# Kernel tuning notes

Measured on AMD Instinct MI355X. Metric: run time of the kernel, lower is better.

The kernel has to match this reference:

```python
import jax, jax.numpy as jnp
from jax import lax
import numpy as np

SHAPE = (50, 60, 65)   # -> after net: (17, 27, 32), flatten = 14688
NEG = 0.01             # LeakyReLU default slope
B, N = 8, 80000        # batch size, total active voxels


def _lrelu(x):
    return jnp.where(x >= 0, x, NEG * x)


def _sparse_conv(x, w, b, m):
    # Regular (non-submanifold) sparse conv == dense VALID conv on densified
    # input (inactive sites are 0 so they contribute nothing). Output site is
    # active iff any input site in the kernel footprint is active; bias is
    # added only at active output sites.
    k = w.shape[2]
    y = lax.conv_general_dilated(x, w, (1, 1, 1), 'VALID',
                                 dimension_numbers=('NCDHW', 'OIDHW', 'NCDHW'))
    m2 = lax.reduce_window(m, 0.0, lax.max, (1, 1, k, k, k), (1, 1, 1, 1, 1), 'VALID')
    y = jnp.where(m2 > 0, y + b[None, :, None, None, None], 0.0)
    return y, m2


def _sparse_maxpool(x, m, k):
    # spconv SparseMaxPool: max over ACTIVE sites only (inactive excluded, not 0)
    xm = jnp.where(m > 0, x, -jnp.inf)
    p = lax.reduce_window(xm, -jnp.inf, lax.max, (1, 1, k, k, k), (1, 1, 1, 1, 1), 'VALID')
    m2 = lax.reduce_window(m, 0.0, lax.max, (1, 1, k, k, k), (1, 1, 1, 1, 1), 'VALID')
    return jnp.where(m2 > 0, p, 0.0), m2


def setup_inputs() -> dict:
    key = jax.random.key(0)
    ks = jax.random.split(key, 24)
    D, H, W = SHAPE
    features = jax.random.normal(ks[0], (N, 1), dtype=jnp.float32)
    bi = jax.random.randint(ks[1], (N,), 0, B)
    zi = jax.random.randint(ks[2], (N,), 0, D)
    yi = jax.random.randint(ks[3], (N,), 0, H)
    xi = jax.random.randint(ks[4], (N,), 0, W)
    coors = jnp.stack([bi, zi, yi, xi], axis=1).astype(jnp.int32)
    s = 0.05
    p = {}
    p['w1'] = jax.random.normal(ks[5], (32, 1, 4, 4, 4), jnp.float32) * s
    p['b1'] = jax.random.normal(ks[6], (32,), jnp.float32) * s
    p['w2'] = jax.random.normal(ks[7], (32, 32, 4, 4, 4), jnp.float32) * s
    p['b2'] = jax.random.normal(ks[8], (32,), jnp.float32) * s
    p['w3'] = jax.random.normal(ks[9], (32, 32, 4, 4, 4), jnp.float32) * s
    p['b3'] = jax.random.normal(ks[10], (32,), jnp.float32) * s
    p['w4'] = jax.random.normal(ks[11], (32, 32, 4, 4, 4), jnp.float32) * s
    p['b4'] = jax.random.normal(ks[12], (32,), jnp.float32) * s
    p['w5'] = jax.random.normal(ks[13], (32, 32, 4, 4, 4), jnp.float32) * s
    p['b5'] = jax.random.normal(ks[14], (32,), jnp.float32) * s
    p['w6'] = jax.random.normal(ks[15], (32, 32, 4, 4, 4), jnp.float32) * s
    p['b6'] = jax.random.normal(ks[16], (32,), jnp.float32) * s
    p['w7'] = jax.random.normal(ks[17], (1, 32, 4, 4, 4), jnp.float32) * s
    p['b7'] = jax.random.normal(ks[18], (1,), jnp.float32) * s
    p['W8'] = jax.random.normal(ks[19], (14688, 1000), jnp.float32) * 0.01
    p['b8'] = jax.random.normal(ks[20], (1000,), jnp.float32) * s
    p['W9'] = jax.random.normal(ks[21], (1000, 1000), jnp.float32) * 0.03
    p['b9'] = jax.random.normal(ks[22], (1000,), jnp.float32) * s
    p['W10'] = jax.random.normal(ks[23], (1000, 1), jnp.float32) * 0.03
    p['b10'] = jnp.zeros((1,), jnp.float32)
    return dict(features=features, coors=coors, batch_size=B, **p)


def reference(features, coors, batch_size,
              w1, b1, w2, b2, w3, b3, w4, b4, w5, b5, w6, b6, w7, b7,
              W8, b8, W9, b9, W10, b10):
    D, H, W = SHAPE
    bi, zi, yi, xi = coors[:, 0], coors[:, 1], coors[:, 2], coors[:, 3]
    dense = jnp.zeros((batch_size, 1, D, H, W), features.dtype)
    dense = dense.at[bi, 0, zi, yi, xi].set(features[:, 0])
    mask = jnp.zeros((batch_size, 1, D, H, W), features.dtype)
    mask = mask.at[bi, 0, zi, yi, xi].set(1.0)

    x, m = _sparse_conv(dense, w1, b1, mask); x = _lrelu(x)
    x, m = _sparse_conv(x, w2, b2, m);        x = _lrelu(x)
    x, m = _sparse_maxpool(x, m, 5)
    x, m = _sparse_conv(x, w3, b3, m);        x = _lrelu(x)
    x, m = _sparse_conv(x, w4, b4, m);        x = _lrelu(x)
    x, m = _sparse_maxpool(x, m, 5)
    x, m = _sparse_conv(x, w5, b5, m);        x = _lrelu(x)
    x, m = _sparse_conv(x, w6, b6, m);        x = _lrelu(x)
    x, m = _sparse_conv(x, w7, b7, m);        x = _lrelu(x)
    x, m = _sparse_maxpool(x, m, 5)

    # ToDense (inactive sites already 0) + Flatten -> [B, 14688]
    h = x.reshape(x.shape[0], -1)
    h = _lrelu(h @ W8 + b8)
    h = _lrelu(h @ W9 + b9)
    out = _lrelu(h @ W10 + b10)
    return out
```

## Files before the change

### kernel.cpp

```cpp
#include <hip/hip_runtime.h>
#include <cstddef>


#define NEGSLOPE 0.01f
#define NINF (-3.0e38f)

#define TZ 4
#define TY 4
#define TXT 16
#define IZ 7
#define IY 7
#define IX 19
#define NV (IZ*IY*IX)

#define CZ 4
#define CY 4
#define CX 8
#define HIY 7
#define HIX 11
#define HNV (7*HIY*HIX)

typedef __attribute__((ext_vector_type(8)))  short  short8;
typedef __attribute__((ext_vector_type(16))) float  floatx16;

__device__ __forceinline__ float lrelu(float v) { return v >= 0.f ? v : NEGSLOPE * v; }

__device__ __forceinline__ unsigned short f2bf(float f) {
  unsigned b = __float_as_uint(f);
  return (unsigned short)((b + 0x7fffu + ((b >> 16) & 1u)) >> 16);
}
__device__ __forceinline__ float bf2f(unsigned short h) {
  return __uint_as_float(((unsigned)h) << 16);
}
__device__ __forceinline__ unsigned splitpair(float a, float b, unsigned& lo) {
  unsigned short ha = f2bf(a), hb = f2bf(b);
  unsigned short la = f2bf(a - bf2f(ha)), lb = f2bf(b - bf2f(hb));
  lo = (unsigned)la | ((unsigned)lb << 16);
  return (unsigned)ha | ((unsigned)hb << 16);
}

__global__ void k_claim(const int* __restrict__ coors, unsigned* __restrict__ claim, int N) {
  int i = blockIdx.x * blockDim.x + threadIdx.x;
  if (i >= N) return;
  int b = coors[4*i], z = coors[4*i+1], y = coors[4*i+2], x = coors[4*i+3];
  int v = ((b*50 + z)*60 + y)*65 + x;
  atomicMax(&claim[v], (unsigned)(i + 1));
}

__global__ void k_scatter(const int* __restrict__ coors, const float* __restrict__ feat,
                          const unsigned* __restrict__ claim,
                          float* __restrict__ x0, float* __restrict__ m0, int N) {
  int i = blockIdx.x * blockDim.x + threadIdx.x;
  if (i >= N) return;
  int b = coors[4*i], z = coors[4*i+1], y = coors[4*i+2], x = coors[4*i+3];
  int v = ((b*50 + z)*60 + y)*65 + x;
  m0[v] = 1.f;
  if (claim[v] == (unsigned)(i + 1)) x0[v] = feat[i];
}

__global__ void k_repack(const float* __restrict__ w, float* __restrict__ wr, int CI, int CO) {
  int i = blockIdx.x * blockDim.x + threadIdx.x;
  int tot = CO * CI * 64;
  if (i >= tot) return;
  int k = i & 63;
  int ci = (i >> 6) % CI;
  int co = i / (64 * CI);
  wr[(k * CI + ci) * CO + co] = w[i];
}

__global__ void k_repack_mfma(const float* __restrict__ w, unsigned short* __restrict__ tbl) {
  int i = blockIdx.x * blockDim.x + threadIdx.x;
  if (i >= 64*4*2*64) return;
  int lane = i & 63; int t = i >> 6;
  int pack = t & 1; t >>= 1;
  int pass = t & 3; int tap = t >> 2;
  int co = lane & 31; int oct = lane >> 5;
#pragma unroll
  for (int j = 0; j < 8; ++j) {
    int k = oct * 8 + j;
    int ci = pass * 8 + (k & 7);
    int part = ((k >> 3) ^ pack) & 1;
    float wv = w[((co * 32 + ci) << 6) + tap];
    unsigned short wh = f2bf(wv);
    unsigned short r = part ? f2bf(wv - bf2f(wh)) : wh;
    tbl[(size_t)i * 8 + j] = r;
  }
}

__global__ void kd_z(const float* __restrict__ in, float* __restrict__ o,
                     int Zi, int Yi, int Xi, int Zo, int K, int nI) {
  int gid = blockIdx.x * blockDim.x + threadIdx.x;
  int perOut = Zo * Yi * Xi;
  if (gid >= nI * perOut) return;
  int item = gid / perOut;
  int r = gid - item * perOut;
  int x = r % Xi; int t = r / Xi;
  int y = t % Yi; int z = t / Yi;
  const float* ib = in + (size_t)item * Zi * Yi * Xi;
  float mx = 0.f;
  for (int d = 0; d < K; d++) mx = fmaxf(mx, ib[((z + d) * Yi + y) * Xi + x]);
  o[gid] = mx;
}

__global__ void kd_y(const float* __restrict__ in, float* __restrict__ o,
                     int Zo, int Yi, int Xi, int Yo, int K, int nI) {
  int gid = blockIdx.x * blockDim.x + threadIdx.x;
  int perOut = Zo * Yo * Xi;
  if (gid >= nI * perOut) return;
  int item = gid / perOut;
  int r = gid - item * perOut;
  int x = r % Xi; int t = r / Xi;
  int y = t % Yo; int z = t / Yo;
  const float* ib = in + (size_t)item * Zo * Yi * Xi;
  float mx = 0.f;
  for (int d = 0; d < K; d++) mx = fmaxf(mx, ib[(z * Yi + y + d) * Xi + x]);
  o[gid] = mx;
}

__global__ void kd_x(const float* __restrict__ in, float* __restrict__ o,
                     int Zo, int Yo, int Xi, int Xo, int K, int nI) {
  int gid = blockIdx.x * blockDim.x + threadIdx.x;
  int perOut = Zo * Yo * Xo;
  if (gid >= nI * perOut) return;
  int item = gid / perOut;
  int r = gid - item * perOut;
  int x = r % Xo; int t = r / Xo;
  int y = t % Yo; int z = t / Yo;
  const float* ib = in + (size_t)item * Zo * Yo * Xi;
  float mx = 0.f;
  for (int d = 0; d < K; d++) mx = fmaxf(mx, ib[(z * Yo + y) * Xi + x + d]);
  o[gid] = mx;
}

__global__ __launch_bounds__(256, 6)
void k_conv32m(const float* __restrict__ in, const unsigned short* __restrict__ tbl,
               const float* __restrict__ bias, const float* __restrict__ mo,
               float* __restrict__ out,
               int Zi, int Yi, int Xi, int Zo, int Yo, int Xo,
               int tilesZ, int tilesY, int tilesX) {
  __shared__ unsigned sU[HNV * 12];
  const int perIn = Zi * Yi * Xi;
  const int perOut = Zo * Yo * Xo;
  int bid = blockIdx.x;
  int txi = bid % tilesX; bid /= tilesX;
  int tyi = bid % tilesY; bid /= tilesY;
  int tzi = bid % tilesZ; int item = bid / tilesZ;
  const int z0 = tzi * CZ, y0 = tyi * CY, x0 = txi * CX;
  const int tid = threadIdx.x;
  const int lane = tid & 63;
  const int col = lane & 31;
  const int oct = lane >> 5;
  const int wv  = tid >> 6;

  const int lvBase = ((wv) * HIY + ((col >> 3) & 3)) * HIX + (col & 7);

  floatx16 acc;
#pragma unroll
  for (int r = 0; r < 16; ++r) acc[r] = 0.f;

  const float* inb = in + (size_t)item * perIn * 32;
  const char* tb = (const char*)tbl + lane * 16;

#pragma unroll 1
  for (int p = 0; p < 4; ++p) {
    __syncthreads();
    for (int idx = tid; idx < HNV; idx += 256) {
      int iz = idx / (HIY * HIX); int r = idx - iz * (HIY * HIX);
      int iy = r / HIX; int ix = r - iy * HIX;
      int gz = z0 + iz, gy = y0 + iy, gx = x0 + ix;
      float4 f0 = make_float4(0.f,0.f,0.f,0.f), f1 = make_float4(0.f,0.f,0.f,0.f);
      if (gz < Zi && gy < Yi && gx < Xi) {
        const float* vp = inb + (size_t)((gz * Yi + gy) * Xi + gx) * 32 + p * 8;
        f0 = *(const float4*)vp;
        f1 = *(const float4*)(vp + 4);
      }
      unsigned l0, l1, l2, l3;
      unsigned h0 = splitpair(f0.x, f0.y, l0);
      unsigned h1 = splitpair(f0.z, f0.w, l1);
      unsigned h2 = splitpair(f1.x, f1.y, l2);
      unsigned h3 = splitpair(f1.z, f1.w, l3);
      uint4 ahv = {h0, h1, h2, h3};
      uint4 alv = {l0, l1, l2, l3};
      ((uint4*)sU)[idx * 3 + 0] = ahv;
      ((uint4*)sU)[idx * 3 + 1] = alv;
    }
    __syncthreads();

    const char* tp = tb + (size_t)p * 2048;
#pragma unroll 2
    for (int tap = 0; tap < 64; ++tap) {
      int kz = tap >> 4, ky = (tap >> 2) & 3, kx = tap & 3;
      int sOff = (kz * HIY + ky) * HIX + kx;
      short8 b0 = *(const short8*)(tp + (size_t)tap * 8192);
      short8 b1 = *(const short8*)(tp + (size_t)tap * 8192 + 1024);
      short8 a0 = *(const short8*)((const char*)sU + (size_t)(lvBase + sOff) * 48 + oct * 16);
      acc = __builtin_amdgcn_mfma_f32_32x32x16_bf16(a0, b0, acc, 0, 0, 0);
      acc = __builtin_amdgcn_mfma_f32_32x32x16_bf16(a0, b1, acc, 0, 0, 0);
    }
  }

  const float bco = bias[col];
#pragma unroll
  for (int rg = 0; rg < 16; ++rg) {
    int row = (rg & 3) + 8 * (rg >> 2) + 4 * oct;
    int oz = wv, oy = (row >> 3) & 3, ox = row & 7;
    int gz = z0 + oz, gy = y0 + oy, gx = x0 + ox;
    if (gz < Zo && gy < Yo && gx < Xo) {
      int ov = item * perOut + (gz * Yo + gy) * Xo + gx;
      bool act = mo[ov] > 0.f;
      out[(size_t)ov * 32 + col] = lrelu(act ? (acc[rg] + bco) : 0.f);
    }
  }
}

__global__ __launch_bounds__(256, 2)
void k_conv1t(const float* __restrict__ in, const float* __restrict__ wr,
              const float* __restrict__ bias, const float* __restrict__ mo,
              float* __restrict__ out,
              int Zi, int Yi, int Xi, int Zo, int Yo, int Xo,
              int tilesZ, int tilesY, int tilesX) {
  __shared__ float sinf[NV];
  __shared__ float4 wsh[512];
  {
    const float4* wr4 = (const float4*)wr;
    for (int idx = threadIdx.x; idx < 512; idx += 256) wsh[idx] = wr4[idx];
  }
  const int perIn = Zi * Yi * Xi;
  const int perOut = Zo * Yo * Xo;
  int bid = blockIdx.x;
  int txi = bid % tilesX; bid /= tilesX;
  int tyi = bid % tilesY; bid /= tilesY;
  int tzi = bid % tilesZ; int item = bid / tilesZ;
  const int z0 = tzi * TZ, y0 = tyi * TY, x0 = txi * TXT;
  const int tid = threadIdx.x;
  const int ox = tid & 15, oy = (tid >> 4) & 3, oz = tid >> 6;

  const float* inb = in + (size_t)item * perIn;
  for (int idx = tid; idx < NV; idx += 256) {
    int iz = idx / (IY * IX); int r = idx - iz * (IY * IX);
    int iy = r / IX; int ix = r - iy * IX;
    int gz = z0 + iz, gy = y0 + iy, gx = x0 + ix;
    float val = 0.f;
    if (gz < Zi && gy < Yi && gx < Xi)
      val = inb[(size_t)((gz * Yi + gy) * Xi + gx)];
    sinf[idx] = val;
  }
  __syncthreads();

  float4 acc[8];
#pragma unroll
  for (int j = 0; j < 8; ++j) acc[j] = make_float4(0.f, 0.f, 0.f, 0.f);

#pragma unroll 1
  for (int tap = 0; tap < 64; ++tap) {
    int kz = tap >> 4, ky = (tap >> 2) & 3, kx = tap & 3;
    int lv = ((oz + kz) * IY + (oy + ky)) * IX + (ox + kx);
    float av = sinf[lv];
#pragma unroll
    for (int j = 0; j < 8; ++j) {
      float4 wvv = wsh[tap * 8 + j];
      acc[j].x = fmaf(av, wvv.x, acc[j].x);
      acc[j].y = fmaf(av, wvv.y, acc[j].y);
      acc[j].z = fmaf(av, wvv.z, acc[j].z);
      acc[j].w = fmaf(av, wvv.w, acc[j].w);
    }
  }

  int gz = z0 + oz, gy = y0 + oy, gx = x0 + ox;
  if (gz < Zo && gy < Yo && gx < Xo) {
    int ov = item * perOut + (gz * Yo + gy) * Xo + gx;
    bool act = mo[ov] > 0.f;
    const float4* b4 = (const float4*)bias;
    float* op = out + (size_t)ov * 32;
#pragma unroll
    for (int j = 0; j < 8; ++j) {
      float4 r = acc[j]; float4 bj = b4[j];
      r.x = lrelu(act ? (r.x + bj.x) : 0.f);
      r.y = lrelu(act ? (r.y + bj.y) : 0.f);
      r.z = lrelu(act ? (r.z + bj.z) : 0.f);
      r.w = lrelu(act ? (r.w + bj.w) : 0.f);
      *(float4*)(op + j * 4) = r;
    }
  }
}

__global__ __launch_bounds__(256, 2)
void k_conv7t(const float* __restrict__ in, const float* __restrict__ wr,
              const float* __restrict__ bias, const float* __restrict__ mo,
              float* __restrict__ out,
              int Zi, int Yi, int Xi, int Zo, int Yo, int Xo,
              int tilesZ, int tilesY, int tilesX) {
  __shared__ float4 sin4[4][NV];
  __shared__ float4 wsh[512];
  {
    const float4* wr4 = (const float4*)wr;
    for (int idx = threadIdx.x; idx < 512; idx += 256) wsh[idx] = wr4[idx];
  }
  const int perIn = Zi * Yi * Xi;
  const int perOut = Zo * Yo * Xo;
  int bid = blockIdx.x;
  int txi = bid % tilesX; bid /= tilesX;
  int tyi = bid % tilesY; bid /= tilesY;
  int tzi = bid % tilesZ; int item = bid / tilesZ;
  const int z0 = tzi * TZ, y0 = tyi * TY, x0 = txi * TXT;
  const int tid = threadIdx.x;
  const int ox = tid & 15, oy = (tid >> 4) & 3, oz = tid >> 6;

  const float* inb = in + (size_t)item * perIn * 32;
  float acc = 0.f;

#pragma unroll 1
  for (int h = 0; h < 2; ++h) {
    __syncthreads();
    for (int idx = tid; idx < NV * 4; idx += 256) {
      int q = idx / NV; int v = idx - q * NV;
      int iz = v / (IY * IX); int r = v - iz * (IY * IX);
      int iy = r / IX; int ix = r - iy * IX;
      int gz = z0 + iz, gy = y0 + iy, gx = x0 + ix;
      float4 val = make_float4(0.f, 0.f, 0.f, 0.f);
      if (gz < Zi && gy < Yi && gx < Xi)
        val = *(const float4*)(inb + (size_t)((gz * Yi + gy) * Xi + gx) * 32 + h * 16 + q * 4);
      sin4[q][v] = val;
    }
    __syncthreads();
#pragma unroll 1
    for (int tap = 0; tap < 64; ++tap) {
      int kz = tap >> 4, ky = (tap >> 2) & 3, kx = tap & 3;
      int lv = ((oz + kz) * IY + (oy + ky)) * IX + (ox + kx);
      float4 a0 = sin4[0][lv];
      float4 a1 = sin4[1][lv];
      float4 a2 = sin4[2][lv];
      float4 a3 = sin4[3][lv];
      float4 w0 = wsh[tap * 8 + h * 4 + 0];
      float4 w1 = wsh[tap * 8 + h * 4 + 1];
      float4 w2 = wsh[tap * 8 + h * 4 + 2];
      float4 w3 = wsh[tap * 8 + h * 4 + 3];
      acc += a0.x*w0.x + a0.y*w0.y + a0.z*w0.z + a0.w*w0.w
           + a1.x*w1.x + a1.y*w1.y + a1.z*w1.z + a1.w*w1.w
           + a2.x*w2.x + a2.y*w2.y + a2.z*w2.z + a2.w*w2.w
           + a3.x*w3.x + a3.y*w3.y + a3.z*w3.z + a3.w*w3.w;
    }
  }

  int gz = z0 + oz, gy = y0 + oy, gx = x0 + ox;
  if (gz < Zo && gy < Yo && gx < Xo) {
    int ov = item * perOut + (gz * Yo + gy) * Xo + gx;
    bool act = mo[ov] > 0.f;
    out[ov] = lrelu(act ? (acc + bias[0]) : 0.f);
  }
}

__global__ void k_pool_z(const float* __restrict__ in, const float* __restrict__ m,
                         float* __restrict__ out, int Zi, int Yi, int Xi, int Zo, int nI) {
  int gid = blockIdx.x * blockDim.x + threadIdx.x;
  int perOut = Zo * Yi * Xi;
  int tot = nI * perOut * 8;
  if (gid >= tot) return;
  int c4 = gid & 7; int v = gid >> 3;
  int item = v / perOut;
  int r = v - item * perOut;
  int x = r % Xi; int t = r / Xi;
  int y = t % Yi; int z = t / Yi;
  int ib = item * Zi * Yi * Xi;
  float4 acc = {NINF, NINF, NINF, NINF};
  for (int j = 0; j < 5; j++) {
    int vi = ib + ((z + j)*Yi + y)*Xi + x;
    if (m[vi] > 0.f) {
      float4 val = *(const float4*)(in + (size_t)vi*32 + c4*4);
      acc.x = fmaxf(acc.x, val.x); acc.y = fmaxf(acc.y, val.y);
      acc.z = fmaxf(acc.z, val.z); acc.w = fmaxf(acc.w, val.w);
    }
  }
  *(float4*)(out + (size_t)v*32 + c4*4) = acc;
}

__global__ void k_pool_y(const float* __restrict__ in, float* __restrict__ out,
                         int Z, int Yi, int Xi, int Yo, int nI) {
  int gid = blockIdx.x * blockDim.x + threadIdx.x;
  int perOut = Z * Yo * Xi;
  int tot = nI * perOut * 8;
  if (gid >= tot) return;
  int c4 = gid & 7; int v = gid >> 3;
  int item = v / perOut;
  int r = v - item * perOut;
  int x = r % Xi; int t = r / Xi;
  int y = t % Yo; int z = t / Yo;
  int ib = item * Z * Yi * Xi;
  float4 acc = {NINF, NINF, NINF, NINF};
  for (int j = 0; j < 5; j++) {
    int vi = ib + (z*Yi + y + j)*Xi + x;
    float4 val = *(const float4*)(in + (size_t)vi*32 + c4*4);
    acc.x = fmaxf(acc.x, val.x); acc.y = fmaxf(acc.y, val.y);
    acc.z = fmaxf(acc.z, val.z); acc.w = fmaxf(acc.w, val.w);
  }
  *(float4*)(out + (size_t)v*32 + c4*4) = acc;
}

__global__ void k_pool_x(const float* __restrict__ in, const float* __restrict__ mp,
                         float* __restrict__ out, int Z, int Y, int Xi, int Xo, int nI) {
  int gid = blockIdx.x * blockDim.x + threadIdx.x;
  int perOut = Z * Y * Xo;
  int tot = nI * perOut * 8;
  if (gid >= tot) return;
  int c4 = gid & 7; int v = gid >> 3;
  int item = v / perOut;
  int r = v - item * perOut;
  int x = r % Xo; int t = r / Xo;
  int y = t % Y; int z = t / Y;
  int ib = item * Z * Y * Xi;
  float4 acc = {NINF, NINF, NINF, NINF};
  for (int j = 0; j < 5; j++) {
    int vi = ib + (z*Y + y)*Xi + x + j;
    float4 val = *(const float4*)(in + (size_t)vi*32 + c4*4);
    acc.x = fmaxf(acc.x, val.x); acc.y = fmaxf(acc.y, val.y);
    acc.z = fmaxf(acc.z, val.z); acc.w = fmaxf(acc.w, val.w);
  }
  bool act = mp[v] > 0.f;
  float4 rr;
  rr.x = act ? acc.x : 0.f; rr.y = act ? acc.y : 0.f;
  rr.z = act ? acc.z : 0.f; rr.w = act ? acc.w : 0.f;
  *(float4*)(out + (size_t)v*32 + c4*4) = rr;
}

__global__ void k_pool3(const float* __restrict__ xin, const float* __restrict__ m,
                        const float* __restrict__ mp, float* __restrict__ out, int nI) {
  int gid = blockIdx.x * blockDim.x + threadIdx.x;
  int perOut = 17 * 27 * 32;
  int tot = nI * perOut;
  if (gid >= tot) return;
  int item = gid / perOut;
  int r = gid - item * perOut;
  int x = r & 31; int t = r >> 5;
  int y = t % 27; int z = t / 27;
  const float* xb = xin + (size_t)item * 23436;
  const float* mb = m + (size_t)item * 23436;
  float acc = NINF;
  for (int dz = 0; dz < 5; dz++)
    for (int dy = 0; dy < 5; dy++) {
      const float* rowx = xb + (size_t)(((z + dz)*31 + y + dy)*36 + x);
      const float* rowm = mb + (size_t)(((z + dz)*31 + y + dy)*36 + x);
      for (int dx = 0; dx < 5; dx++)
        if (rowm[dx] > 0.f) acc = fmaxf(acc, rowx[dx]);
    }
  out[gid] = (mp[gid] > 0.f) ? acc : 0.f;
}

__global__ __launch_bounds__(256, 4)
void k_fc_part(const float* __restrict__ X, const float* __restrict__ Wm,
               float* __restrict__ part, int K, int Ncol, int Kc) {
  __shared__ float sm[16][16][8];
  int ks = blockIdx.y;
  int k0 = ks * Kc;
  int k1 = k0 + Kc; if (k1 > K) k1 = K;
  int cl = threadIdx.x & 15;
  int kt = threadIdx.x >> 4;
  int col = blockIdx.x * 16 + cl;
  float a0=0.f,a1=0.f,a2=0.f,a3=0.f,a4=0.f,a5=0.f,a6=0.f,a7=0.f;
  if (col < Ncol) {
    for (int k = k0 + kt; k < k1; k += 16) {
      float w = Wm[(size_t)k * Ncol + col];
      a0 += X[0 * K + k] * w; a1 += X[1 * K + k] * w;
      a2 += X[2 * K + k] * w; a3 += X[3 * K + k] * w;
      a4 += X[4 * K + k] * w; a5 += X[5 * K + k] * w;
      a6 += X[6 * K + k] * w; a7 += X[7 * K + k] * w;
    }
  }
  sm[kt][cl][0]=a0; sm[kt][cl][1]=a1; sm[kt][cl][2]=a2; sm[kt][cl][3]=a3;
  sm[kt][cl][4]=a4; sm[kt][cl][5]=a5; sm[kt][cl][6]=a6; sm[kt][cl][7]=a7;
  __syncthreads();
  if (threadIdx.x < 128) {
    int c = threadIdx.x & 15;
    int b = threadIdx.x >> 4;
    float s = 0.f;
#pragma unroll
    for (int k = 0; k < 16; k++) s += sm[k][c][b];
    int cc = blockIdx.x * 16 + c;
    if (cc < Ncol) part[((size_t)ks * 8 + b) * Ncol + cc] = s;
  }
}

__global__ void k_fc_fin(const float* __restrict__ part, int ns,
                         const float* __restrict__ bias, float* __restrict__ out, int Ncol) {
  int i = blockIdx.x * blockDim.x + threadIdx.x;
  if (i >= 8 * Ncol) return;
  int b = i / Ncol;
  int c = i - b * Ncol;
  float s = 0.f;
  for (int ks = 0; ks < ns; ks++) s += part[((size_t)ks * 8 + b) * Ncol + c];
  out[i] = lrelu(s + bias[c]);
}

__global__ __launch_bounds__(256, 4)
void k_fc(const float* __restrict__ X, const float* __restrict__ Wm,
          const float* __restrict__ bias, float* __restrict__ out,
          int K, int Ncol) {
  __shared__ float sm[16][16][8];
  int cl = threadIdx.x & 15;
  int kt = threadIdx.x >> 4;
  int col = blockIdx.x * 16 + cl;
  float a0=0.f,a1=0.f,a2=0.f,a3=0.f,a4=0.f,a5=0.f,a6=0.f,a7=0.f;
  if (col < Ncol) {
    for (int k = kt; k < K; k += 16) {
      float w = Wm[(size_t)k * Ncol + col];
      a0 += X[0 * K + k] * w; a1 += X[1 * K + k] * w;
      a2 += X[2 * K + k] * w; a3 += X[3 * K + k] * w;
      a4 += X[4 * K + k] * w; a5 += X[5 * K + k] * w;
      a6 += X[6 * K + k] * w; a7 += X[7 * K + k] * w;
    }
  }
  sm[kt][cl][0]=a0; sm[kt][cl][1]=a1; sm[kt][cl][2]=a2; sm[kt][cl][3]=a3;
  sm[kt][cl][4]=a4; sm[kt][cl][5]=a5; sm[kt][cl][6]=a6; sm[kt][cl][7]=a7;
  __syncthreads();
  if (threadIdx.x < 128) {
    int c = threadIdx.x & 15;
    int b = threadIdx.x >> 4;
    float s = 0.f;
#pragma unroll
    for (int k = 0; k < 16; k++) s += sm[k][c][b];
    int cc = blockIdx.x * 16 + c;
    if (cc < Ncol) out[b * Ncol + cc] = lrelu(s + bias[cc]);
  }
}

static inline int G256(long long n) { return (int)((n + 255) / 256); }

extern "C" void kernel_launch(void* const* d_in, const int* in_sizes, int n_in,
                              void* d_out, int out_size, void* d_ws, size_t ws_size,
                              hipStream_t stream) {
  const float* feat  = (const float*)d_in[0];
  const int*   coors = (const int*)d_in[1];
  const float* w1 = (const float*)d_in[3];  const float* b1 = (const float*)d_in[4];
  const float* w2 = (const float*)d_in[5];  const float* b2 = (const float*)d_in[6];
  const float* w3 = (const float*)d_in[7];  const float* b3 = (const float*)d_in[8];
  const float* w4 = (const float*)d_in[9];  const float* b4 = (const float*)d_in[10];
  const float* w5 = (const float*)d_in[11]; const float* b5 = (const float*)d_in[12];
  const float* w6 = (const float*)d_in[13]; const float* b6 = (const float*)d_in[14];
  const float* w7 = (const float*)d_in[15]; const float* b7 = (const float*)d_in[16];
  const float* W8 = (const float*)d_in[17]; const float* b8 = (const float*)d_in[18];
  const float* W9 = (const float*)d_in[19]; const float* b9 = (const float*)d_in[20];
  const float* W10= (const float*)d_in[21]; const float* b10= (const float*)d_in[22];
  float* out = (float*)d_out;

  char* ws = (char*)d_ws;
  size_t off = 0;
  auto alloc = [&](size_t nfloats) -> float* {
    float* p = (float*)(ws + off);
    off += ((nfloats * 4 + 1023) / 1024) * 1024;
    return p;
  };

  float* x0  = alloc(1560000);
  float* m0  = alloc(1560000);
  float* m1  = alloc(8 * 166098);
  float* m2  = alloc(8 * 140184);
  float* mp1 = alloc(8 * 110000);
  float* m3  = alloc(8 * 90428);
  float* m4  = alloc(8 * 73304);
  float* mp2 = alloc(8 * 54000);
  float* m5  = alloc(8 * 41958);
  float* m6  = alloc(8 * 31824);
  float* m7  = alloc(8 * 23436);
  float* mp3 = alloc(8 * 14688);
  float* p3  = alloc(8 * 14688);
  float* dt1 = alloc(8 * 183300);
  float* dt2 = alloc(8 * 174135);
  float* wr1 = alloc(2048);
  float* wr7 = alloc(2048);
  unsigned short* tb2 = (unsigned short*)alloc(131072);
  unsigned short* tb3 = (unsigned short*)alloc(131072);
  unsigned short* tb4 = (unsigned short*)alloc(131072);
  unsigned short* tb5 = (unsigned short*)alloc(131072);
  unsigned short* tb6 = (unsigned short*)alloc(131072);
  float* part= alloc(64000);
  float* h8  = alloc(8000);
  float* h9  = alloc(8000);
  size_t fixedOff = off;

  const size_t perItemAB = ((size_t)5315136*4 + 1023)/1024*1024
                         + ((size_t)4485888*4 + 1023)/1024*1024
                         + ((size_t)23436*4 + 1023)/1024*1024;
  int G = 0;
  for (int g : {8, 4, 2, 1})
    if (fixedOff + (size_t)g * perItemAB <= ws_size) { G = g; break; }
  if (G == 0) return;

  float* A  = alloc((size_t)G * 5315136);
  float* Bb = alloc((size_t)G * 4485888);
  float* x7 = alloc((size_t)G * 23436);
  unsigned* claim = (unsigned*)A;

  hipMemsetAsync(claim, 0, 1560000 * 4, stream);
  hipMemsetAsync(x0,    0, 1560000 * 4, stream);
  hipMemsetAsync(m0,    0, 1560000 * 4, stream);

  k_repack<<<G256(32*1*64),  256, 0, stream>>>(w1, wr1, 1, 32);
  k_repack<<<G256(1*32*64),  256, 0, stream>>>(w7, wr7, 32, 1);
  k_repack_mfma<<<128, 256, 0, stream>>>(w2, tb2);
  k_repack_mfma<<<128, 256, 0, stream>>>(w3, tb3);
  k_repack_mfma<<<128, 256, 0, stream>>>(w4, tb4);
  k_repack_mfma<<<128, 256, 0, stream>>>(w5, tb5);
  k_repack_mfma<<<128, 256, 0, stream>>>(w6, tb6);

  const int N = 80000;
  k_claim  <<<G256(N), 256, 0, stream>>>(coors, claim, N);
  k_scatter<<<G256(N), 256, 0, stream>>>(coors, feat, claim, x0, m0, N);

  auto dil3 = [&](const float* src, float* dst,
                  int Zi, int Yi, int Xi, int Zo, int Yo, int Xo, int K) {
    kd_z<<<G256((long long)8*Zo*Yi*Xi), 256, 0, stream>>>(src, dt1, Zi,Yi,Xi, Zo, K, 8);
    kd_y<<<G256((long long)8*Zo*Yo*Xi), 256, 0, stream>>>(dt1, dt2, Zo,Yi,Xi, Yo, K, 8);
    kd_x<<<G256((long long)8*Zo*Yo*Xo), 256, 0, stream>>>(dt2, dst, Zo,Yo,Xi, Xo, K, 8);
  };
  dil3(m0,  m1,  50,60,65, 47,57,62, 4);
  dil3(m1,  m2,  47,57,62, 44,54,59, 4);
  dil3(m2,  mp1, 44,54,59, 40,50,55, 5);
  dil3(mp1, m3,  40,50,55, 37,47,52, 4);
  dil3(m3,  m4,  37,47,52, 34,44,49, 4);
  dil3(m4,  mp2, 34,44,49, 30,40,45, 5);
  dil3(mp2, m5,  30,40,45, 27,37,42, 4);
  dil3(m5,  m6,  27,37,42, 24,34,39, 4);
  dil3(m6,  m7,  24,34,39, 21,31,36, 4);
  dil3(m7,  mp3, 21,31,36, 17,27,32, 5);

  auto conv32 = [&](const float* in, const unsigned short* tbl, const float* bias,
                    const float* mo, float* o,
                    int Zi, int Yi, int Xi, int Zo, int Yo, int Xo, int nI) {
    int tz = (Zo + CZ - 1) / CZ, ty = (Yo + CY - 1) / CY, tx = (Xo + CX - 1) / CX;
    k_conv32m<<<nI * tz * ty * tx, 256, 0, stream>>>(
        in, tbl, bias, mo, o, Zi, Yi, Xi, Zo, Yo, Xo, tz, ty, tx);
  };

  for (int g0 = 0; g0 < 8; g0 += G) {
    const float* x0g  = x0  + (size_t)g0 * 195000;
    const float* m1g  = m1  + (size_t)g0 * 166098;
    const float* m2g  = m2  + (size_t)g0 * 140184;
    const float* mp1g = mp1 + (size_t)g0 * 110000;
    const float* m3g  = m3  + (size_t)g0 * 90428;
    const float* m4g  = m4  + (size_t)g0 * 73304;
    const float* mp2g = mp2 + (size_t)g0 * 54000;
    const float* m5g  = m5  + (size_t)g0 * 41958;
    const float* m6g  = m6  + (size_t)g0 * 31824;
    const float* m7g  = m7  + (size_t)g0 * 23436;
    const float* mp3g = mp3 + (size_t)g0 * 14688;

    {
      int tz = (47 + TZ - 1) / TZ, ty = (57 + TY - 1) / TY, tx = (62 + TXT - 1) / TXT;
      k_conv1t<<<G * tz * ty * tx, 256, 0, stream>>>(
          x0g, wr1, b1, m1g, A, 50,60,65, 47,57,62, tz, ty, tx);
    }
    conv32(A, tb2, b2, m2g, Bb, 47,57,62, 44,54,59, G);
    k_pool_z<<<G256((long long)G*127440*8), 256, 0, stream>>>(Bb, m2g,  A,  44,54,59, 40, G);
    k_pool_y<<<G256((long long)G*118000*8), 256, 0, stream>>>(A,  Bb, 40,54,59, 50, G);
    k_pool_x<<<G256((long long)G*110000*8), 256, 0, stream>>>(Bb, mp1g, A,  40,50,59, 55, G);
    conv32(A, tb3, b3, m3g, Bb, 40,50,55, 37,47,52, G);
    conv32(Bb, tb4, b4, m4g, A, 37,47,52, 34,44,49, G);
    k_pool_z<<<G256((long long)G*64680*8), 256, 0, stream>>>(A,  m4g,  Bb, 34,44,49, 30, G);
    k_pool_y<<<G256((long long)G*58800*8), 256, 0, stream>>>(Bb, A,  30,44,49, 40, G);
    k_pool_x<<<G256((long long)G*54000*8), 256, 0, stream>>>(A,  mp2g, Bb, 30,40,49, 45, G);
    conv32(Bb, tb5, b5, m5g, A, 30,40,45, 27,37,42, G);
    conv32(A, tb6, b6, m6g, Bb, 27,37,42, 24,34,39, G);
    {
      int tz = (21 + TZ - 1) / TZ, ty = (31 + TY - 1) / TY, tx = (36 + TXT - 1) / TXT;
      k_conv7t<<<G * tz * ty * tx, 256, 0, stream>>>(
          Bb, wr7, b7, m7g, x7, 24,34,39, 21,31,36, tz, ty, tx);
    }
    k_pool3<<<G256((long long)G*14688), 256, 0, stream>>>(
        x7, m7g, mp3g, p3 + (size_t)g0 * 14688, G);
  }

  k_fc_part<<<dim3(63, 8), 256, 0, stream>>>(p3, W8, part, 14688, 1000, 1836);
  k_fc_fin <<<G256(8000), 256, 0, stream>>>(part, 8, b8, h8, 1000);
  k_fc_part<<<dim3(63, 4), 256, 0, stream>>>(h8, W9, part, 1000, 1000, 250);
  k_fc_fin <<<G256(8000), 256, 0, stream>>>(part, 4, b9, h9, 1000);
  k_fc<<<1, 256, 0, stream>>>(h9, W10, b10, out, 1000, 1);
}
```

Before: 3.574 ms.

## Double output tile per block in MFMA conv, reuse B fragments across two accumulators

The 32-channel conv kernel now covers a 4x4x16 output tile per block instead of 4x4x8. Each wave holds two 32-row accumulators, so each loaded weight fragment feeds four MFMAs instead of two. The shared-memory stride per voxel drops from 48 to 40 bytes, written and read as uint2 pairs to cut padding and bank conflicts. The goal is less redundant halo loading and bf16 splitting per output, and more MFMA work per weight load, at the cost of more registers (occupancy hint lowered from 6 to 4) and more wasted tiles at the X edges.

```diff
diff --git a/kernel.cpp b/kernel.cpp
--- a/kernel.cpp
+++ b/kernel.cpp
@@ -13,15 +13,9 @@
 #define IX 19
 #define NV (IZ*IY*IX)
 
-#define CZ 4
-#define CY 4
-#define CX 8
-#define HIY 7
-#define HIX 11
-#define HNV (7*HIY*HIX)
-
-typedef __attribute__((ext_vector_type(8)))  short  short8;
-typedef __attribute__((ext_vector_type(16))) float  floatx16;
+typedef __attribute__((ext_vector_type(8)))  short    short8;
+typedef __attribute__((ext_vector_type(4)))  unsigned uint4v;
+typedef __attribute__((ext_vector_type(16))) float    floatx16;
 
 __device__ __forceinline__ float lrelu(float v) { return v >= 0.f ? v : NEGSLOPE * v; }
 
@@ -37,6 +31,13 @@
   unsigned short la = f2bf(a - bf2f(ha)), lb = f2bf(b - bf2f(hb));
   lo = (unsigned)la | ((unsigned)lb << 16);
   return (unsigned)ha | ((unsigned)hb << 16);
+}
+
+__device__ __forceinline__ short8 ld_frag(const uint2* s2, int v, int oct) {
+  uint2 u0 = s2[v * 5 + oct * 2];
+  uint2 u1 = s2[v * 5 + oct * 2 + 1];
+  uint4v t; t.x = u0.x; t.y = u0.y; t.z = u1.x; t.w = u1.y;
+  return __builtin_bit_cast(short8, t);
 }
 
 __global__ void k_claim(const int* __restrict__ coors, unsigned* __restrict__ claim, int N) {
@@ -132,41 +133,48 @@
   o[gid] = mx;
 }
 
-__global__ __launch_bounds__(256, 6)
+__global__ __launch_bounds__(256, 4)
 void k_conv32m(const float* __restrict__ in, const unsigned short* __restrict__ tbl,
                const float* __restrict__ bias, const float* __restrict__ mo,
                float* __restrict__ out,
                int Zi, int Yi, int Xi, int Zo, int Yo, int Xo,
                int tilesZ, int tilesY, int tilesX) {
-  __shared__ unsigned sU[HNV * 12];
+  __shared__ unsigned sU[NV * 10];
   const int perIn = Zi * Yi * Xi;
   const int perOut = Zo * Yo * Xo;
   int bid = blockIdx.x;
   int txi = bid % tilesX; bid /= tilesX;
   int tyi = bid % tilesY; bid /= tilesY;
   int tzi = bid % tilesZ; int item = bid / tilesZ;
-  const int z0 = tzi * CZ, y0 = tyi * CY, x0 = txi * CX;
+  const int z0 = tzi * TZ, y0 = tyi * TY, x0 = txi * TXT;
   const int tid = threadIdx.x;
   const int lane = tid & 63;
   const int col = lane & 31;
   const int oct = lane >> 5;
   const int wv  = tid >> 6;
 
-  const int lvBase = ((wv) * HIY + ((col >> 3) & 3)) * HIX + (col & 7);
-
-  floatx16 acc;
-#pragma unroll
-  for (int r = 0; r < 16; ++r) acc[r] = 0.f;
+  int lvBase0, lvBase1;
+  {
+    int vt0 = (2*wv + 0)*32 + col;
+    int vt1 = (2*wv + 1)*32 + col;
+    lvBase0 = ((vt0 >> 6)*IY + ((vt0 >> 4) & 3))*IX + (vt0 & 15);
+    lvBase1 = ((vt1 >> 6)*IY + ((vt1 >> 4) & 3))*IX + (vt1 & 15);
+  }
+
+  floatx16 acc0, acc1;
+#pragma unroll
+  for (int r = 0; r < 16; ++r) { acc0[r] = 0.f; acc1[r] = 0.f; }
 
   const float* inb = in + (size_t)item * perIn * 32;
   const char* tb = (const char*)tbl + lane * 16;
+  uint2* s2 = (uint2*)sU;
 
 #pragma unroll 1
   for (int p = 0; p < 4; ++p) {
     __syncthreads();
-    for (int idx = tid; idx < HNV; idx += 256) {
-      int iz = idx / (HIY * HIX); int r = idx - iz * (HIY * HIX);
-      int iy = r / HIX; int ix = r - iy * HIX;
+    for (int idx = tid; idx < NV; idx += 256) {
+      int iz = idx / (IY * IX); int r = idx - iz * (IY * IX);
+      int iy = r / IX; int ix = r - iy * IX;
       int gz = z0 + iz, gy = y0 + iy, gx = x0 + ix;
       float4 f0 = make_float4(0.f,0.f,0.f,0.f), f1 = make_float4(0.f,0.f,0.f,0.f);
       if (gz < Zi && gy < Yi && gx < Xi) {
@@ -179,10 +187,10 @@
       unsigned h1 = splitpair(f0.z, f0.w, l1);
       unsigned h2 = splitpair(f1.x, f1.y, l2);
       unsigned h3 = splitpair(f1.z, f1.w, l3);
-      uint4 ahv = {h0, h1, h2, h3};
-      uint4 alv = {l0, l1, l2, l3};
-      ((uint4*)sU)[idx * 3 + 0] = ahv;
-      ((uint4*)sU)[idx * 3 + 1] = alv;
+      s2[idx * 5 + 0] = make_uint2(h0, h1);
+      s2[idx * 5 + 1] = make_uint2(h2, h3);
+      s2[idx * 5 + 2] = make_uint2(l0, l1);
+      s2[idx * 5 + 3] = make_uint2(l2, l3);
     }
     __syncthreads();
 
@@ -190,25 +198,34 @@
 #pragma unroll 2
     for (int tap = 0; tap < 64; ++tap) {
       int kz = tap >> 4, ky = (tap >> 2) & 3, kx = tap & 3;
-      int sOff = (kz * HIY + ky) * HIX + kx;
+      int sOff = (kz * IY + ky) * IX + kx;
       short8 b0 = *(const short8*)(tp + (size_t)tap * 8192);
       short8 b1 = *(const short8*)(tp + (size_t)tap * 8192 + 1024);
-      short8 a0 = *(const short8*)((const char*)sU + (size_t)(lvBase + sOff) * 48 + oct * 16);
-      acc = __builtin_amdgcn_mfma_f32_32x32x16_bf16(a0, b0, acc, 0, 0, 0);
-      acc = __builtin_amdgcn_mfma_f32_32x32x16_bf16(a0, b1, acc, 0, 0, 0);
+      short8 a0 = ld_frag(s2, lvBase0 + sOff, oct);
+      short8 a1 = ld_frag(s2, lvBase1 + sOff, oct);
+      acc0 = __builtin_amdgcn_mfma_f32_32x32x16_bf16(a0, b0, acc0, 0, 0, 0);
+      acc0 = __builtin_amdgcn_mfma_f32_32x32x16_bf16(a0, b1, acc0, 0, 0, 0);
+      acc1 = __builtin_amdgcn_mfma_f32_32x32x16_bf16(a1, b0, acc1, 0, 0, 0);
+      acc1 = __builtin_amdgcn_mfma_f32_32x32x16_bf16(a1, b1, acc1, 0, 0, 0);
     }
   }
 
   const float bco = bias[col];
 #pragma unroll
-  for (int rg = 0; rg < 16; ++rg) {
-    int row = (rg & 3) + 8 * (rg >> 2) + 4 * oct;
-    int oz = wv, oy = (row >> 3) & 3, ox = row & 7;
-    int gz = z0 + oz, gy = y0 + oy, gx = x0 + ox;
-    if (gz < Zo && gy < Yo && gx < Xo) {
-      int ov = item * perOut + (gz * Yo + gy) * Xo + gx;
-      bool act = mo[ov] > 0.f;
-      out[(size_t)ov * 32 + col] = lrelu(act ? (acc[rg] + bco) : 0.f);
+  for (int gg = 0; gg < 2; ++gg) {
+    int vtb = (2*wv + gg) * 32;
+#pragma unroll
+    for (int rg = 0; rg < 16; ++rg) {
+      int row = (rg & 3) + 8 * (rg >> 2) + 4 * oct;
+      int vt = vtb + row;
+      int oz = vt >> 6, oy = (vt >> 4) & 3, ox = vt & 15;
+      int gz = z0 + oz, gy = y0 + oy, gx = x0 + ox;
+      if (gz < Zo && gy < Yo && gx < Xo) {
+        int ov = item * perOut + (gz * Yo + gy) * Xo + gx;
+        float val = (gg == 0) ? acc0[rg] : acc1[rg];
+        bool act = mo[ov] > 0.f;
+        out[(size_t)ov * 32 + col] = lrelu(act ? (val + bco) : 0.f);
+      }
     }
   }
 }
@@ -625,7 +642,7 @@
   auto conv32 = [&](const float* in, const unsigned short* tbl, const float* bias,
                     const float* mo, float* o,
                     int Zi, int Yi, int Xi, int Zo, int Yo, int Xo, int nI) {
-    int tz = (Zo + CZ - 1) / CZ, ty = (Yo + CY - 1) / CY, tx = (Xo + CX - 1) / CX;
+    int tz = (Zo + TZ - 1) / TZ, ty = (Yo + TY - 1) / TY, tx = (Xo + TXT - 1) / TXT;
     k_conv32m<<<nI * tz * ty * tx, 256, 0, stream>>>(
         in, tbl, bias, mo, o, Zi, Yi, Xi, Zo, Yo, Xo, tz, ty, tx);
   };
```

After: 3.321 ms. 1.08x faster.
